# Kernel tuning notes

Hardware: AMD Instinct MI355X
Metric: run time of the kernel (lower is better)

Reference implementation:

```python
import jax, jax.numpy as jnp
import numpy as np

NF = 128  # latent_dim / number of filters


def setup_inputs() -> dict:
    key = jax.random.key(0)
    k1, k2, k3, k4 = jax.random.split(key, 4)
    B, H, W, C = 4, 64, 64, 128
    x = jax.random.normal(k1, (B, H, W, C), dtype=jnp.float32)
    y = jax.random.normal(k2, (B, H, W, C), dtype=jnp.float32)
    # 1x1 conv kernels (C_in, C_out) + biases, glorot-ish scale
    scale = 1.0 / np.sqrt(C)
    W1 = jax.random.normal(k3, (C, NF), dtype=jnp.float32) * scale
    W2 = jax.random.normal(k4, (C, NF), dtype=jnp.float32) * scale
    b1 = jnp.zeros((NF,), dtype=jnp.float32)
    b2 = jnp.zeros((NF,), dtype=jnp.float32)
    return {"x": x, "y": y, "W1": W1, "b1": b1, "W2": W2, "b2": b2}


def reference(x, y, W1, b1, W2, b2):
    B, H, Wd, C = x.shape
    hw = H * Wd
    # 1x1 convs == per-pixel matmul
    xq = jnp.einsum('bhwc,cf->bhwf', x, W1) + b1   # conv1(x)
    yk = jnp.einsum('bhwc,cf->bhwf', y, W2) + b2   # conv2(y)
    xq_r = xq.reshape(B, hw, NF)
    yk_r = yk.reshape(B, hw, NF)
    # A_ij = sigmoid(y_i . x_j), full (hw x hw) sigmoid attention
    A = jax.nn.sigmoid(jnp.einsum('bic,bjc->bij', yk_r, xq_r))
    out = jnp.einsum('bij,bjc->bic', A, yk_r).reshape(B, H, Wd, NF)
    # residual add of the *projected* x (matches original: x was overwritten by conv1)
    out = out + xq
    return out
```

## Files before the change

### kernel.cpp

```cpp
#include <hip/hip_runtime.h>
#include <hip/hip_bf16.h>
#include <stdint.h>

typedef float f32x16 __attribute__((ext_vector_type(16)));
typedef float f32x4  __attribute__((ext_vector_type(4)));
typedef short s16x8  __attribute__((ext_vector_type(8)));
typedef unsigned int u32x4 __attribute__((ext_vector_type(4)));

#define HWSZ   4096
#define NBATCH 4
#define LOG2E  1.44269504088896340736f

__device__ __forceinline__ unsigned short f2bf(float f) {
    unsigned u = __builtin_bit_cast(unsigned, f);
    u += 0x7FFFu + ((u >> 16) & 1u);
    return (unsigned short)(u >> 16);
}
__device__ __forceinline__ unsigned cvt_pk_bf16(float lo, float hi) {
    __hip_bfloat162 h = __float22bfloat162_rn(make_float2(lo, hi));
    return *reinterpret_cast<unsigned*>(&h);
}

__global__ __launch_bounds__(256, 1) void proj_kernel(
    const float* __restrict__ x, const float* __restrict__ y,
    const float* __restrict__ W1, const float* __restrict__ b1,
    const float* __restrict__ W2, const float* __restrict__ b2,
    float* __restrict__ xq_f32,
    unsigned short* __restrict__ xq_bf,
    unsigned short* __restrict__ yk_bf,
    unsigned short* __restrict__ ykT_bf)
{
    __shared__ unsigned short Xlds[64][136];
    __shared__ unsigned short Ylds[64][136];
    __shared__ unsigned short Tlds[128][72];

    const int t    = threadIdx.x;
    const int lane = t & 63;
    const int w    = t >> 6;
    const int l31  = lane & 31;
    const int g    = lane >> 5;
    const int r0   = blockIdx.x * 64;
    const int b    = r0 >> 12;
    const int j0   = r0 & (HWSZ - 1);

    #pragma unroll
    for (int i = 0; i < 8; ++i) {
        int li = t + 256 * i;
        int row = li >> 5, c = (li & 31) * 4;
        float4 vx = *(const float4*)(x + (size_t)(r0 + row) * 128 + c);
        float4 vy = *(const float4*)(y + (size_t)(r0 + row) * 128 + c);
        *(uint2*)&Xlds[row][c] = make_uint2(cvt_pk_bf16(vx.x, vx.y), cvt_pk_bf16(vx.z, vx.w));
        *(uint2*)&Ylds[row][c] = make_uint2(cvt_pk_bf16(vy.x, vy.y), cvt_pk_bf16(vy.z, vy.w));
    }
    __syncthreads();

    const int m  = w >> 1;
    const int fh = w & 1;
    const float* Wm = m ? W2 : W1;
    const float* bm = m ? b2 : b1;
    const unsigned short* A0 = m ? &Ylds[0][0] : &Xlds[0][0];

    f32x16 acc[2][2];
    #pragma unroll
    for (int i = 0; i < 16; ++i) {
        acc[0][0][i] = 0.f; acc[0][1][i] = 0.f;
        acc[1][0][i] = 0.f; acc[1][1][i] = 0.f;
    }

    #pragma unroll
    for (int ks = 0; ks < 8; ++ks) {
        s16x8 bfr[2];
        #pragma unroll
        for (int ft = 0; ft < 2; ++ft) {
            const float* wp = Wm + (size_t)(ks * 16 + g * 8) * 128 + fh * 64 + ft * 32 + l31;
            #pragma unroll
            for (int i = 0; i < 8; ++i)
                bfr[ft][i] = (short)f2bf(wp[(size_t)i * 128]);
        }
        #pragma unroll
        for (int rt = 0; rt < 2; ++rt) {
            s16x8 af = *(const s16x8*)(A0 + (size_t)(rt * 32 + l31) * 136 + ks * 16 + g * 8);
            acc[rt][0] = __builtin_amdgcn_mfma_f32_32x32x16_bf16(af, bfr[0], acc[rt][0], 0, 0, 0);
            acc[rt][1] = __builtin_amdgcn_mfma_f32_32x32x16_bf16(af, bfr[1], acc[rt][1], 0, 0, 0);
        }
    }

    const float bias_v[2] = { bm[fh * 64 + l31], bm[fh * 64 + 32 + l31] };

    if (m == 0) {
        #pragma unroll
        for (int rt = 0; rt < 2; ++rt)
        #pragma unroll
        for (int ft = 0; ft < 2; ++ft) {
            int f = fh * 64 + ft * 32 + l31;
            #pragma unroll
            for (int r = 0; r < 16; ++r) {
                int row = rt * 32 + (r & 3) + 8 * (r >> 2) + 4 * g;
                float v = acc[rt][ft][r] + bias_v[ft];
                size_t o = (size_t)(r0 + row) * 128 + f;
                xq_f32[o] = v;
                xq_bf[o]  = f2bf(v * LOG2E);
            }
        }
    } else {
        #pragma unroll
        for (int rt = 0; rt < 2; ++rt)
        #pragma unroll
        for (int ft = 0; ft < 2; ++ft) {
            int f = fh * 64 + ft * 32 + l31;
            #pragma unroll
            for (int rg = 0; rg < 4; ++rg) {
                float p0 = acc[rt][ft][4 * rg + 0] + bias_v[ft];
                float p1 = acc[rt][ft][4 * rg + 1] + bias_v[ft];
                float p2 = acc[rt][ft][4 * rg + 2] + bias_v[ft];
                float p3 = acc[rt][ft][4 * rg + 3] + bias_v[ft];
                int jb = rt * 32 + 8 * rg + 4 * g;
                *(uint2*)&Tlds[f][jb] = make_uint2(cvt_pk_bf16(p0, p1), cvt_pk_bf16(p2, p3));
                size_t o = (size_t)(r0 + jb) * 128 + f;
                yk_bf[o]       = f2bf(p0);
                yk_bf[o + 128] = f2bf(p1);
                yk_bf[o + 256] = f2bf(p2);
                yk_bf[o + 384] = f2bf(p3);
            }
        }
    }
    __syncthreads();

    {
        int f  = t >> 1;
        int jh = (t & 1) * 32;
        unsigned short* dst = ykT_bf + ((size_t)(b * 128 + f)) * HWSZ + j0 + jh;
        #pragma unroll
        for (int c = 0; c < 4; ++c)
            *(s16x8*)(dst + c * 8) = *(const s16x8*)&Tlds[f][jh + c * 8];
    }
}

#define KT_STR   136
#define VT_STR   72
#define KT_BYTES (64 * KT_STR * 2)
#define VT_BYTES (128 * VT_STR * 2)
#define BUF_BYTES (KT_BYTES + VT_BYTES)

__global__ __launch_bounds__(256, 2) void attn128_kernel(
    const unsigned short* __restrict__ Kbf,
    const unsigned short* __restrict__ Qbf,
    const unsigned short* __restrict__ Vtbf,
    float* __restrict__ outp)
{
    __shared__ __align__(16) char smem[2 * BUF_BYTES];

    const int t    = threadIdx.x;
    const int lane = t & 63;
    const int qt   = t >> 6;
    const int l31  = lane & 31;
    const int g    = lane >> 5;

    const int split = blockIdx.x >> 7;
    const int r     = blockIdx.x & 127;
    const int b     = r >> 5;
    const int qb    = (r & 31) * 128;
    const int jBegin = split * (HWSZ / 4);
    const int nt     = (HWSZ / 4) / 64;

    s16x8 qfrag[8];
    {
        const unsigned short* qp =
            Qbf + (((size_t)(b * HWSZ + qb + 32 * qt + l31)) << 7) + g * 8;
        #pragma unroll
        for (int fs = 0; fs < 8; ++fs)
            qfrag[fs] = *(const s16x8*)(qp + fs * 16);
    }

    f32x16 acc[4];
    #pragma unroll
    for (int ft = 0; ft < 4; ++ft)
        #pragma unroll
        for (int i = 0; i < 16; ++i) acc[ft][i] = 0.f;

    const unsigned short* Kbase = Kbf  + (((size_t)b * HWSZ) << 7);
    const unsigned short* Vbase = Vtbf + (((size_t)b) << 7) * HWSZ;

    const unsigned short* kSrc = Kbase + (size_t)(jBegin + (t >> 4)) * 128 + (t & 15) * 8;
    const unsigned short* vSrc = Vbase + (size_t)(t >> 3) * HWSZ + jBegin + (t & 7) * 8;
    const int kDst = (t >> 4) * KT_STR + (t & 15) * 8;
    const int vDst = (t >> 3) * VT_STR + (t & 7) * 8;

    {
        unsigned short* Kl = (unsigned short*)smem;
        unsigned short* Vl = (unsigned short*)(smem + KT_BYTES);
        #pragma unroll
        for (int i = 0; i < 4; ++i)
            *(s16x8*)(Kl + kDst + i * 16 * KT_STR) = *(const s16x8*)(kSrc + (size_t)i * 2048);
        #pragma unroll
        for (int i = 0; i < 4; ++i)
            *(s16x8*)(Vl + vDst + i * 32 * VT_STR) = *(const s16x8*)(vSrc + (size_t)i * 32 * HWSZ);
    }
    __syncthreads();

    int c = 0;
    for (int it = 0; it < nt; ++it) {
        const bool pre = (it + 1 < nt);
        s16x8 kr[4], vr[4];
        if (pre) {
            kSrc += 64 * 128;
            vSrc += 64;
            #pragma unroll
            for (int i = 0; i < 4; ++i)
                kr[i] = *(const s16x8*)(kSrc + (size_t)i * 2048);
            #pragma unroll
            for (int i = 0; i < 4; ++i)
                vr[i] = *(const s16x8*)(vSrc + (size_t)i * 32 * HWSZ);
        }

        const unsigned short* Kl = (const unsigned short*)(smem + c * BUF_BYTES);
        const unsigned short* Vl = (const unsigned short*)(smem + c * BUF_BYTES + KT_BYTES);

        #pragma unroll
        for (int jt = 0; jt < 2; ++jt) {
            f32x16 sa, sb;
            #pragma unroll
            for (int i = 0; i < 16; ++i) { sa[i] = 0.f; sb[i] = 0.f; }
            const unsigned short* Krow = Kl + (size_t)(32 * jt + l31) * KT_STR + g * 8;
            __builtin_amdgcn_s_setprio(1);
            #pragma unroll
            for (int fs = 0; fs < 4; ++fs) {
                sa = __builtin_amdgcn_mfma_f32_32x32x16_bf16(
                         *(const s16x8*)(Krow + fs * 16), qfrag[fs], sa, 0, 0, 0);
                sb = __builtin_amdgcn_mfma_f32_32x32x16_bf16(
                         *(const s16x8*)(Krow + (fs + 4) * 16), qfrag[fs + 4], sb, 0, 0, 0);
            }
            __builtin_amdgcn_s_setprio(0);

            unsigned W0[4], W1[4];
            #pragma unroll
            for (int rg = 0; rg < 4; ++rg) {
                float s0 = sa[4 * rg + 0] + sb[4 * rg + 0];
                float s1 = sa[4 * rg + 1] + sb[4 * rg + 1];
                float s2v = sa[4 * rg + 2] + sb[4 * rg + 2];
                float s3 = sa[4 * rg + 3] + sb[4 * rg + 3];
                float p0 = __builtin_amdgcn_rcpf(1.f + __builtin_amdgcn_exp2f(-s0));
                float p1 = __builtin_amdgcn_rcpf(1.f + __builtin_amdgcn_exp2f(-s1));
                float p2 = __builtin_amdgcn_rcpf(1.f + __builtin_amdgcn_exp2f(-s2v));
                float p3 = __builtin_amdgcn_rcpf(1.f + __builtin_amdgcn_exp2f(-s3));
                W0[rg] = cvt_pk_bf16(p0, p1);
                W1[rg] = cvt_pk_bf16(p2, p3);
            }

            #pragma unroll
            for (int s2 = 0; s2 < 2; ++s2) {
                unsigned o0 = g ? W0[2 * s2 + 1] : W0[2 * s2];
                unsigned o1 = g ? W1[2 * s2 + 1] : W1[2 * s2];
                unsigned t0 = g ? W0[2 * s2]     : W0[2 * s2 + 1];
                unsigned t1 = g ? W1[2 * s2]     : W1[2 * s2 + 1];
                unsigned r0 = __shfl_xor(t0, 32, 64);
                unsigned r1 = __shfl_xor(t1, 32, 64);
                u32x4 pw;
                pw[0] = g ? r0 : o0;
                pw[1] = g ? r1 : o1;
                pw[2] = g ? o0 : r0;
                pw[3] = g ? o1 : r1;
                s16x8 pf = __builtin_bit_cast(s16x8, pw);
                const int ks = 2 * jt + s2;
                __builtin_amdgcn_s_setprio(1);
                #pragma unroll
                for (int ft = 0; ft < 4; ++ft) {
                    s16x8 vf = *(const s16x8*)(Vl + (size_t)(32 * ft + l31) * VT_STR + ks * 16 + g * 8);
                    acc[ft] = __builtin_amdgcn_mfma_f32_32x32x16_bf16(pf, vf, acc[ft], 0, 0, 0);
                }
                __builtin_amdgcn_s_setprio(0);
            }
        }

        if (pre) {
            unsigned short* Kd = (unsigned short*)(smem + (c ^ 1) * BUF_BYTES);
            unsigned short* Vd = (unsigned short*)(smem + (c ^ 1) * BUF_BYTES + KT_BYTES);
            #pragma unroll
            for (int i = 0; i < 4; ++i)
                *(s16x8*)(Kd + kDst + i * 16 * KT_STR) = kr[i];
            #pragma unroll
            for (int i = 0; i < 4; ++i)
                *(s16x8*)(Vd + vDst + i * 32 * VT_STR) = vr[i];
        }
        __syncthreads();
        c ^= 1;
    }

    float* op = outp + (size_t)split * ((size_t)NBATCH * HWSZ * 128);
    #pragma unroll
    for (int ft = 0; ft < 4; ++ft)
    #pragma unroll
    for (int r2 = 0; r2 < 16; ++r2) {
        int row = (r2 & 3) + 8 * (r2 >> 2) + 4 * g;
        int q = qb + 32 * qt + row;
        size_t o = (((size_t)(b * HWSZ + q)) << 7) + 32 * ft + l31;
        op[o] = acc[ft][r2];
    }
}

template<bool SPLIT>
__global__ __launch_bounds__(256, 2) void attn_kernel(
    const unsigned short* __restrict__ Kbf,
    const unsigned short* __restrict__ Qbf,
    const unsigned short* __restrict__ Vtbf,
    const float* __restrict__ resid,
    float* __restrict__ outp)
{
    __shared__ __align__(16) char smem[2 * BUF_BYTES];

    const int t    = threadIdx.x;
    const int lane = t & 63;
    const int w    = t >> 6;
    const int qt   = w & 1;
    const int jt   = w >> 1;
    const int l31  = lane & 31;
    const int g    = lane >> 5;

    int bid = blockIdx.x;
    int half = 0;
    if (SPLIT) { half = bid >> 8; bid &= 255; }
    const int b      = bid >> 6;
    const int qb     = (bid & 63) * 64;
    const int jBegin = half * (HWSZ / 2);
    const int nt     = (SPLIT ? HWSZ / 2 : HWSZ) / 64;

    s16x8 qfrag[8];
    {
        const unsigned short* qp =
            Qbf + (((size_t)(b * HWSZ + qb + 32 * qt + l31)) << 7) + g * 8;
        #pragma unroll
        for (int fs = 0; fs < 8; ++fs)
            qfrag[fs] = *(const s16x8*)(qp + fs * 16);
    }

    f32x16 acc[4];
    #pragma unroll
    for (int ft = 0; ft < 4; ++ft)
        #pragma unroll
        for (int i = 0; i < 16; ++i) acc[ft][i] = 0.f;

    const unsigned short* Kbase = Kbf  + (((size_t)b * HWSZ) << 7);
    const unsigned short* Vbase = Vtbf + (((size_t)b) << 7) * HWSZ;

    const unsigned short* kSrc = Kbase + (size_t)(jBegin + (t >> 4)) * 128 + (t & 15) * 8;
    const unsigned short* vSrc = Vbase + (size_t)(t >> 3) * HWSZ + jBegin + (t & 7) * 8;
    const int kDst = (t >> 4) * KT_STR + (t & 15) * 8;
    const int vDst = (t >> 3) * VT_STR + (t & 7) * 8;

    {
        unsigned short* Kl = (unsigned short*)smem;
        unsigned short* Vl = (unsigned short*)(smem + KT_BYTES);
        #pragma unroll
        for (int i = 0; i < 4; ++i)
            *(s16x8*)(Kl + kDst + i * 16 * KT_STR) = *(const s16x8*)(kSrc + (size_t)i * 2048);
        #pragma unroll
        for (int i = 0; i < 4; ++i)
            *(s16x8*)(Vl + vDst + i * 32 * VT_STR) = *(const s16x8*)(vSrc + (size_t)i * 32 * HWSZ);
    }
    __syncthreads();

    int c = 0;
    for (int it = 0; it < nt; ++it) {
        const bool pre = (it + 1 < nt);
        s16x8 kr[4], vr[4];
        if (pre) {
            kSrc += 64 * 128;
            vSrc += 64;
            #pragma unroll
            for (int i = 0; i < 4; ++i)
                kr[i] = *(const s16x8*)(kSrc + (size_t)i * 2048);
            #pragma unroll
            for (int i = 0; i < 4; ++i)
                vr[i] = *(const s16x8*)(vSrc + (size_t)i * 32 * HWSZ);
        }

        const unsigned short* Kl = (const unsigned short*)(smem + c * BUF_BYTES);
        const unsigned short* Vl = (const unsigned short*)(smem + c * BUF_BYTES + KT_BYTES);

        f32x16 sa, sb;
        #pragma unroll
        for (int i = 0; i < 16; ++i) { sa[i] = 0.f; sb[i] = 0.f; }
        const unsigned short* Krow = Kl + (size_t)(32 * jt + l31) * KT_STR + g * 8;
        __builtin_amdgcn_s_setprio(1);
        #pragma unroll
        for (int fs = 0; fs < 4; ++fs) {
            sa = __builtin_amdgcn_mfma_f32_32x32x16_bf16(
                     *(const s16x8*)(Krow + fs * 16), qfrag[fs], sa, 0, 0, 0);
            sb = __builtin_amdgcn_mfma_f32_32x32x16_bf16(
                     *(const s16x8*)(Krow + (fs + 4) * 16), qfrag[fs + 4], sb, 0, 0, 0);
        }
        __builtin_amdgcn_s_setprio(0);

        unsigned W0[4], W1[4];
        #pragma unroll
        for (int rg = 0; rg < 4; ++rg) {
            float s0 = sa[4 * rg + 0] + sb[4 * rg + 0];
            float s1 = sa[4 * rg + 1] + sb[4 * rg + 1];
            float s2v = sa[4 * rg + 2] + sb[4 * rg + 2];
            float s3 = sa[4 * rg + 3] + sb[4 * rg + 3];
            float p0 = __builtin_amdgcn_rcpf(1.f + __builtin_amdgcn_exp2f(-s0));
            float p1 = __builtin_amdgcn_rcpf(1.f + __builtin_amdgcn_exp2f(-s1));
            float p2 = __builtin_amdgcn_rcpf(1.f + __builtin_amdgcn_exp2f(-s2v));
            float p3 = __builtin_amdgcn_rcpf(1.f + __builtin_amdgcn_exp2f(-s3));
            W0[rg] = cvt_pk_bf16(p0, p1);
            W1[rg] = cvt_pk_bf16(p2, p3);
        }

        #pragma unroll
        for (int s2 = 0; s2 < 2; ++s2) {
            unsigned o0 = g ? W0[2 * s2 + 1] : W0[2 * s2];
            unsigned o1 = g ? W1[2 * s2 + 1] : W1[2 * s2];
            unsigned t0 = g ? W0[2 * s2]     : W0[2 * s2 + 1];
            unsigned t1 = g ? W1[2 * s2]     : W1[2 * s2 + 1];
            unsigned r0 = __shfl_xor(t0, 32, 64);
            unsigned r1 = __shfl_xor(t1, 32, 64);
            u32x4 pw;
            pw[0] = g ? r0 : o0;
            pw[1] = g ? r1 : o1;
            pw[2] = g ? o0 : r0;
            pw[3] = g ? o1 : r1;
            s16x8 pf = __builtin_bit_cast(s16x8, pw);
            const int ks = 2 * jt + s2;
            __builtin_amdgcn_s_setprio(1);
            #pragma unroll
            for (int ft = 0; ft < 4; ++ft) {
                s16x8 vf = *(const s16x8*)(Vl + (size_t)(32 * ft + l31) * VT_STR + ks * 16 + g * 8);
                acc[ft] = __builtin_amdgcn_mfma_f32_32x32x16_bf16(pf, vf, acc[ft], 0, 0, 0);
            }
            __builtin_amdgcn_s_setprio(0);
        }

        if (pre) {
            unsigned short* Kd = (unsigned short*)(smem + (c ^ 1) * BUF_BYTES);
            unsigned short* Vd = (unsigned short*)(smem + (c ^ 1) * BUF_BYTES + KT_BYTES);
            #pragma unroll
            for (int i = 0; i < 4; ++i)
                *(s16x8*)(Kd + kDst + i * 16 * KT_STR) = kr[i];
            #pragma unroll
            for (int i = 0; i < 4; ++i)
                *(s16x8*)(Vd + vDst + i * 32 * VT_STR) = vr[i];
        }
        __syncthreads();
        c ^= 1;
    }

    float* red = (float*)smem;
    if (jt == 1) {
        #pragma unroll
        for (int ft = 0; ft < 4; ++ft)
        #pragma unroll
        for (int r = 0; r < 16; ++r) {
            int row = (r & 3) + 8 * (r >> 2) + 4 * g;
            red[qt * 4096 + row * 128 + 32 * ft + l31] = acc[ft][r];
        }
    }
    __syncthreads();
    if (jt == 0) {
        float* op = outp + (SPLIT ? (size_t)half * ((size_t)NBATCH * HWSZ * 128) : 0);
        #pragma unroll
        for (int ft = 0; ft < 4; ++ft)
        #pragma unroll
        for (int r = 0; r < 16; ++r) {
            int row = (r & 3) + 8 * (r >> 2) + 4 * g;
            float v = acc[ft][r] + red[qt * 4096 + row * 128 + 32 * ft + l31];
            int q = qb + 32 * qt + row;
            size_t o = (((size_t)(b * HWSZ + q)) << 7) + 32 * ft + l31;
            if (SPLIT) op[o] = v;
            else       op[o] = v + resid[o];
        }
    }
}

__global__ __launch_bounds__(256, 1) void reduce2_kernel(
    const float* __restrict__ p0, const float* __restrict__ p1, float* outp)
{
    int i = blockIdx.x * 256 + threadIdx.x;
    f32x4 a = ((const f32x4*)p0)[i];
    f32x4 b = ((const f32x4*)p1)[i];
    f32x4 c = ((f32x4*)outp)[i];
    ((f32x4*)outp)[i] = a + b + c;
}

__global__ __launch_bounds__(256, 1) void reduce4_kernel(
    const float* __restrict__ parts, float* __restrict__ outp)
{
    const size_t NELEM4 = (size_t)NBATCH * HWSZ * 128 / 4;
    size_t i = (size_t)blockIdx.x * 256 + threadIdx.x;
    f32x4 a = ((const f32x4*)parts)[i];
    f32x4 b = ((const f32x4*)parts)[i + NELEM4];
    f32x4 c = ((const f32x4*)parts)[i + 2 * NELEM4];
    f32x4 d = ((const f32x4*)parts)[i + 3 * NELEM4];
    f32x4 e = ((f32x4*)outp)[i];
    ((f32x4*)outp)[i] = (a + b) + (c + d) + e;
}

extern "C" void kernel_launch(void* const* d_in, const int* in_sizes, int n_in,
                              void* d_out, int out_size, void* d_ws, size_t ws_size,
                              hipStream_t stream) {
    const float* x  = (const float*)d_in[0];
    const float* y  = (const float*)d_in[1];
    const float* W1 = (const float*)d_in[2];
    const float* b1 = (const float*)d_in[3];
    const float* W2 = (const float*)d_in[4];
    const float* b2 = (const float*)d_in[5];
    float* out = (float*)d_out;

    const size_t NELEM = (size_t)NBATCH * HWSZ * 128;
    unsigned short* xq_bf  = (unsigned short*)d_ws;
    unsigned short* yk_bf  = xq_bf + NELEM;
    unsigned short* ykT_bf = yk_bf + NELEM;
    float* part = (float*)(ykT_bf + NELEM);

    proj_kernel<<<(int)(NBATCH * HWSZ / 64), 256, 0, stream>>>(
        x, y, W1, b1, W2, b2, out, xq_bf, yk_bf, ykT_bf);

    if (ws_size >= NELEM * (6 + 16)) {
        attn128_kernel<<<512, 256, 0, stream>>>(xq_bf, yk_bf, ykT_bf, part);
        reduce4_kernel<<<(int)(NELEM / 1024), 256, 0, stream>>>(part, out);
    } else if (ws_size >= NELEM * (6 + 8)) {
        attn_kernel<true><<<512, 256, 0, stream>>>(xq_bf, yk_bf, ykT_bf, out, part);
        reduce2_kernel<<<(int)(NELEM / 1024), 256, 0, stream>>>(part, part + NELEM, out);
    } else {
        attn_kernel<false><<<256, 256, 0, stream>>>(xq_bf, yk_bf, ykT_bf, out, out);
    }
}
```

Measured before the change: 70.68 us.

## Load K fragments directly from global, keep only V in LDS, add 8-way split

The attention kernel no longer stages K tiles in shared memory. Each wave reads its K MFMA fragments straight from global/L2 into registers, and only V^T is double-buffered in LDS. That shrinks LDS per block, and launch bounds rise to 4 blocks per CU for more occupancy. A templated split count adds an 8-way key split with 1024 blocks when the workspace allows it, plus a generic N-way reduction. The trade-off is redundant global K reads across the four waves with no LDS reuse, and doubled partial-sum traffic in the reduction.

Measured after the change: 229.6 us. 225% more time.

```diff
diff --git a/kernel.cpp b/kernel.cpp
--- a/kernel.cpp
+++ b/kernel.cpp
@@ -142,13 +142,14 @@
 #define VT_BYTES (128 * VT_STR * 2)
 #define BUF_BYTES (KT_BYTES + VT_BYTES)
 
-__global__ __launch_bounds__(256, 2) void attn128_kernel(
+template<int SPLITS>
+__global__ __launch_bounds__(256, 4) void attn128v2_kernel(
     const unsigned short* __restrict__ Kbf,
     const unsigned short* __restrict__ Qbf,
     const unsigned short* __restrict__ Vtbf,
     float* __restrict__ outp)
 {
-    __shared__ __align__(16) char smem[2 * BUF_BYTES];
+    __shared__ __align__(16) unsigned short Vlds[2][128 * VT_STR];
 
     const int t    = threadIdx.x;
     const int lane = t & 63;
@@ -156,12 +157,12 @@
     const int l31  = lane & 31;
     const int g    = lane >> 5;
 
-    const int split = blockIdx.x >> 7;
-    const int r     = blockIdx.x & 127;
-    const int b     = r >> 5;
-    const int qb    = (r & 31) * 128;
-    const int jBegin = split * (HWSZ / 4);
-    const int nt     = (HWSZ / 4) / 64;
+    const int split  = blockIdx.x >> 7;
+    const int r      = blockIdx.x & 127;
+    const int b      = r >> 5;
+    const int qb     = (r & 31) * 128;
+    const int jBegin = split * (HWSZ / SPLITS);
+    const int nt     = (HWSZ / SPLITS) / 64;
 
     s16x8 qfrag[8];
     {
@@ -181,54 +182,48 @@
     const unsigned short* Kbase = Kbf  + (((size_t)b * HWSZ) << 7);
     const unsigned short* Vbase = Vtbf + (((size_t)b) << 7) * HWSZ;
 
-    const unsigned short* kSrc = Kbase + (size_t)(jBegin + (t >> 4)) * 128 + (t & 15) * 8;
+    const unsigned short* kIt = Kbase + (size_t)(jBegin + l31) * 128 + g * 8;
+
     const unsigned short* vSrc = Vbase + (size_t)(t >> 3) * HWSZ + jBegin + (t & 7) * 8;
-    const int kDst = (t >> 4) * KT_STR + (t & 15) * 8;
     const int vDst = (t >> 3) * VT_STR + (t & 7) * 8;
 
     {
-        unsigned short* Kl = (unsigned short*)smem;
-        unsigned short* Vl = (unsigned short*)(smem + KT_BYTES);
         #pragma unroll
         for (int i = 0; i < 4; ++i)
-            *(s16x8*)(Kl + kDst + i * 16 * KT_STR) = *(const s16x8*)(kSrc + (size_t)i * 2048);
-        #pragma unroll
-        for (int i = 0; i < 4; ++i)
-            *(s16x8*)(Vl + vDst + i * 32 * VT_STR) = *(const s16x8*)(vSrc + (size_t)i * 32 * HWSZ);
+            *(s16x8*)(&Vlds[0][0] + vDst + i * 32 * VT_STR) =
+                *(const s16x8*)(vSrc + (size_t)i * 32 * HWSZ);
     }
     __syncthreads();
 
     int c = 0;
     for (int it = 0; it < nt; ++it) {
         const bool pre = (it + 1 < nt);
-        s16x8 kr[4], vr[4];
+        s16x8 vr[4];
         if (pre) {
-            kSrc += 64 * 128;
             vSrc += 64;
-            #pragma unroll
-            for (int i = 0; i < 4; ++i)
-                kr[i] = *(const s16x8*)(kSrc + (size_t)i * 2048);
             #pragma unroll
             for (int i = 0; i < 4; ++i)
                 vr[i] = *(const s16x8*)(vSrc + (size_t)i * 32 * HWSZ);
         }
 
-        const unsigned short* Kl = (const unsigned short*)(smem + c * BUF_BYTES);
-        const unsigned short* Vl = (const unsigned short*)(smem + c * BUF_BYTES + KT_BYTES);
+        const unsigned short* Vl = &Vlds[c][0];
 
         #pragma unroll
         for (int jt = 0; jt < 2; ++jt) {
+            const unsigned short* kp = kIt + jt * 32 * 128;
+            s16x8 kf[8];
+            #pragma unroll
+            for (int fs = 0; fs < 8; ++fs)
+                kf[fs] = *(const s16x8*)(kp + fs * 16);
+
             f32x16 sa, sb;
             #pragma unroll
             for (int i = 0; i < 16; ++i) { sa[i] = 0.f; sb[i] = 0.f; }
-            const unsigned short* Krow = Kl + (size_t)(32 * jt + l31) * KT_STR + g * 8;
             __builtin_amdgcn_s_setprio(1);
             #pragma unroll
             for (int fs = 0; fs < 4; ++fs) {
-                sa = __builtin_amdgcn_mfma_f32_32x32x16_bf16(
-                         *(const s16x8*)(Krow + fs * 16), qfrag[fs], sa, 0, 0, 0);
-                sb = __builtin_amdgcn_mfma_f32_32x32x16_bf16(
-                         *(const s16x8*)(Krow + (fs + 4) * 16), qfrag[fs + 4], sb, 0, 0, 0);
+                sa = __builtin_amdgcn_mfma_f32_32x32x16_bf16(kf[fs], qfrag[fs], sa, 0, 0, 0);
+                sb = __builtin_amdgcn_mfma_f32_32x32x16_bf16(kf[fs + 4], qfrag[fs + 4], sb, 0, 0, 0);
             }
             __builtin_amdgcn_s_setprio(0);
 
@@ -271,16 +266,12 @@
                 __builtin_amdgcn_s_setprio(0);
             }
         }
+        kIt += 64 * 128;
 
         if (pre) {
-            unsigned short* Kd = (unsigned short*)(smem + (c ^ 1) * BUF_BYTES);
-            unsigned short* Vd = (unsigned short*)(smem + (c ^ 1) * BUF_BYTES + KT_BYTES);
             #pragma unroll
             for (int i = 0; i < 4; ++i)
-                *(s16x8*)(Kd + kDst + i * 16 * KT_STR) = kr[i];
-            #pragma unroll
-            for (int i = 0; i < 4; ++i)
-                *(s16x8*)(Vd + vDst + i * 32 * VT_STR) = vr[i];
+                *(s16x8*)(&Vlds[c ^ 1][0] + vDst + i * 32 * VT_STR) = vr[i];
         }
         __syncthreads();
         c ^= 1;
@@ -481,17 +472,17 @@
     ((f32x4*)outp)[i] = a + b + c;
 }
 
-__global__ __launch_bounds__(256, 1) void reduce4_kernel(
+template<int S>
+__global__ __launch_bounds__(256, 1) void reduceN_kernel(
     const float* __restrict__ parts, float* __restrict__ outp)
 {
-    const size_t NELEM4 = (size_t)NBATCH * HWSZ * 128 / 4;
+    const size_t N4 = (size_t)NBATCH * HWSZ * 128 / 4;
     size_t i = (size_t)blockIdx.x * 256 + threadIdx.x;
-    f32x4 a = ((const f32x4*)parts)[i];
-    f32x4 b = ((const f32x4*)parts)[i + NELEM4];
-    f32x4 c = ((const f32x4*)parts)[i + 2 * NELEM4];
-    f32x4 d = ((const f32x4*)parts)[i + 3 * NELEM4];
-    f32x4 e = ((f32x4*)outp)[i];
-    ((f32x4*)outp)[i] = (a + b) + (c + d) + e;
+    f32x4 s = ((f32x4*)outp)[i];
+    #pragma unroll
+    for (int k = 0; k < S; ++k)
+        s += ((const f32x4*)parts)[i + (size_t)k * N4];
+    ((f32x4*)outp)[i] = s;
 }
 
 extern "C" void kernel_launch(void* const* d_in, const int* in_sizes, int n_in,
@@ -514,9 +505,12 @@
     proj_kernel<<<(int)(NBATCH * HWSZ / 64), 256, 0, stream>>>(
         x, y, W1, b1, W2, b2, out, xq_bf, yk_bf, ykT_bf);
 
-    if (ws_size >= NELEM * (6 + 16)) {
-        attn128_kernel<<<512, 256, 0, stream>>>(xq_bf, yk_bf, ykT_bf, part);
-        reduce4_kernel<<<(int)(NELEM / 1024), 256, 0, stream>>>(part, out);
+    if (ws_size >= NELEM * (6 + 32)) {
+        attn128v2_kernel<8><<<1024, 256, 0, stream>>>(xq_bf, yk_bf, ykT_bf, part);
+        reduceN_kernel<8><<<(int)(NELEM / 1024), 256, 0, stream>>>(part, out);
+    } else if (ws_size >= NELEM * (6 + 16)) {
+        attn128v2_kernel<4><<<512, 256, 0, stream>>>(xq_bf, yk_bf, ykT_bf, part);
+        reduceN_kernel<4><<<(int)(NELEM / 1024), 256, 0, stream>>>(part, out);
     } else if (ws_size >= NELEM * (6 + 8)) {
         attn_kernel<true><<<512, 256, 0, stream>>>(xq_bf, yk_bf, ykT_bf, out, part);
         reduce2_kernel<<<(int)(NELEM / 1024), 256, 0, stream>>>(part, part + NELEM, out);
```
